# Kernel tuning notes

Hardware: AMD Instinct MI355X
Metric: run time of the kernel (lower is better)

Reference implementation:

```python
import jax, jax.numpy as jnp
import numpy as np

HIDDEN_DIM = 4096
NUM_EXPERTS = 64
TOP_K = 2
TEMPERATURE = 1.0
NUM_TOKENS = 16384


def setup_inputs() -> dict:
    key = jax.random.key(0)
    kx, kw = jax.random.split(key)
    x = jax.random.normal(kx, (NUM_TOKENS, HIDDEN_DIM), dtype=jnp.float32)
    # nn.Linear(hidden_dim, num_experts, bias=False): weight shape [num_experts, hidden_dim]
    W = jax.random.normal(kw, (NUM_EXPERTS, HIDDEN_DIM), dtype=jnp.float32) * (1.0 / np.sqrt(HIDDEN_DIM))
    return {"x": x, "W": W}


def reference(x, W):
    # gate linear: [N, H] @ [H, E] -> [N, E]
    logits = jnp.einsum("nh,eh->ne", x, W) / TEMPERATURE
    probs = jax.nn.softmax(logits, axis=-1)

    top_k_probs, top_k_indices = jax.lax.top_k(probs, TOP_K)  # [N, k]
    top_k_weights = top_k_probs / jnp.sum(top_k_probs, axis=-1, keepdims=True)

    # ---- stats (fused histogram instead of per-expert loop) ----
    expert_counts = jnp.zeros((NUM_EXPERTS,), dtype=jnp.float32).at[top_k_indices.ravel()].add(1.0)
    avg_probs = jnp.mean(probs, axis=0)
    entropy = jnp.mean(-jnp.sum(probs * jnp.log(probs + 1e-10), axis=-1))
    sorted_counts = jnp.sort(expert_counts)
    n = NUM_EXPERTS
    index = jnp.arange(1, n + 1, dtype=jnp.float32)
    gini = jnp.sum((2.0 * index - n - 1.0) * sorted_counts) / (n * jnp.sum(sorted_counts) + 1e-10)

    return (top_k_indices, top_k_weights, expert_counts, avg_probs, entropy, gini)
```

## Files before the change

### kernel.cpp

```cpp
#include <hip/hip_runtime.h>
#include <cstdint>
#include <cstddef>

#define NTOK 16384
#define HID  4096
#define NEXP 64
#define LO_SCALE 2048.0f
#define LO_INV   (1.0f/2048.0f)

typedef _Float16 half8  __attribute__((ext_vector_type(8)));
typedef _Float16 half4v __attribute__((ext_vector_type(4)));
typedef float    f32x4  __attribute__((ext_vector_type(4)));

__global__ __launch_bounds__(256) void wsplit_kernel(
    const float* __restrict__ W, _Float16* __restrict__ whi,
    _Float16* __restrict__ wlo) {
  int i = (blockIdx.x * 256 + threadIdx.x) * 4;
  float4 w = *(const float4*)(W + i);
  float f[4] = {w.x, w.y, w.z, w.w};
  half4v h, l;
#pragma unroll
  for (int j = 0; j < 4; ++j) {
    float hf = __uint_as_float(__float_as_uint(f[j]) & 0xffffe000u);
    h[j] = (_Float16)hf;
    l[j] = (_Float16)((f[j] - hf) * LO_SCALE);
  }
  *(half4v*)(whi + i) = h;
  *(half4v*)(wlo + i) = l;
}

__global__ __launch_bounds__(256, 2) void fused_kernel(
    const float* __restrict__ x, const _Float16* __restrict__ whi,
    const _Float16* __restrict__ wlo, float* __restrict__ out,
    float* __restrict__ gstats) {
  __shared__ float red[32][NEXP];
  __shared__ float savg[NEXP];
  __shared__ float scnt[NEXP];
  __shared__ float sent;

  const int tid     = threadIdx.x;
  const int lane    = tid & 63;
  const int wv      = tid >> 6;
  const int tokhalf = wv & 1;
  const int khalf   = wv >> 1;
  const int row     = lane & 15;
  const int g       = lane >> 4;

  if (tid < NEXP) { savg[tid] = 0.f; scnt[tid] = 0.f; }
  if (tid == 0) sent = 0.f;

  const int t0 = blockIdx.x * 32 + tokhalf * 16;
  const float*    xp  = x   + (size_t)(t0 + row) * HID + khalf * 2048 + g * 8;
  const _Float16* whp = whi + (size_t)row * HID        + khalf * 2048 + g * 8;
  const _Float16* wlp = wlo + (size_t)row * HID        + khalf * 2048 + g * 8;
  const size_t estride = (size_t)16 * HID;

  f32x4 acc[4], crs[4];
#pragma unroll
  for (int e = 0; e < 4; ++e) {
    acc[e] = (f32x4){0.f, 0.f, 0.f, 0.f};
    crs[e] = (f32x4){0.f, 0.f, 0.f, 0.f};
  }

#define LDA(KS, P0, P1)                              \
  P0 = *(const float4*)(xp + (KS) * 32);             \
  P1 = *(const float4*)(xp + (KS) * 32 + 4);

#define LDB(KS, BH, BL)                                        \
  _Pragma("unroll")                                            \
  for (int e = 0; e < 4; ++e) {                                \
    BH[e] = *(const half8*)(whp + e * estride + (KS) * 32);    \
    BL[e] = *(const half8*)(wlp + e * estride + (KS) * 32);    \
  }

#define STEP(P0, P1, BH, BL)                                              \
  {                                                                       \
    float ff[8] = {P0.x, P0.y, P0.z, P0.w, P1.x, P1.y, P1.z, P1.w};       \
    half8 ah, al;                                                         \
    _Pragma("unroll")                                                     \
    for (int j = 0; j < 8; ++j) {                                         \
      float hf = __uint_as_float(__float_as_uint(ff[j]) & 0xffffe000u);   \
      ah[j] = (_Float16)hf;                                               \
      al[j] = (_Float16)((ff[j] - hf) * LO_SCALE);                        \
    }                                                                     \
    _Pragma("unroll")                                                     \
    for (int e = 0; e < 4; ++e) {                                         \
      acc[e] = __builtin_amdgcn_mfma_f32_16x16x32_f16(ah, BH[e], acc[e], 0, 0, 0); \
      crs[e] = __builtin_amdgcn_mfma_f32_16x16x32_f16(ah, BL[e], crs[e], 0, 0, 0); \
      crs[e] = __builtin_amdgcn_mfma_f32_16x16x32_f16(al, BH[e], crs[e], 0, 0, 0); \
    }                                                                     \
  }

  float4 xa0, xa1, xb0, xb1;
  half8 bh0[4], bl0[4], bh1[4], bl1[4];

  LDA(0, xa0, xa1)
  LDB(0, bh0, bl0)
  for (int ks = 0; ks < 64; ks += 2) {
    LDA(ks + 1, xb0, xb1)
    LDB(ks + 1, bh1, bl1)
    STEP(xa0, xa1, bh0, bl0)
    if (ks + 2 < 64) {
      LDA(ks + 2, xa0, xa1)
      LDB(ks + 2, bh0, bl0)
    }
    STEP(xb0, xb1, bh1, bl1)
  }

  float v[4][4];
#pragma unroll
  for (int e = 0; e < 4; ++e)
#pragma unroll
    for (int r = 0; r < 4; ++r)
      v[e][r] = acc[e][r] + crs[e][r] * LO_INV;

  if (khalf == 1) {
#pragma unroll
    for (int e = 0; e < 4; ++e)
#pragma unroll
      for (int r = 0; r < 4; ++r)
        red[tokhalf * 16 + g * 4 + r][e * 16 + row] = v[e][r];
  }
  __syncthreads();

  if (khalf == 0) {
#pragma unroll
    for (int e = 0; e < 4; ++e)
#pragma unroll
      for (int r = 0; r < 4; ++r)
        v[e][r] += red[tokhalf * 16 + g * 4 + r][e * 16 + row];

    float m[4], S[4], PL[4];
#pragma unroll
    for (int r = 0; r < 4; ++r) {
      float mm = fmaxf(fmaxf(v[0][r], v[1][r]), fmaxf(v[2][r], v[3][r]));
#pragma unroll
      for (int off = 1; off < 16; off <<= 1) mm = fmaxf(mm, __shfl_xor(mm, off));
      m[r] = mm;
    }
    float p[4][4];
#pragma unroll
    for (int e = 0; e < 4; ++e)
#pragma unroll
      for (int r = 0; r < 4; ++r)
        p[e][r] = __expf(v[e][r] - m[r]);
#pragma unroll
    for (int r = 0; r < 4; ++r) {
      float s  = p[0][r] + p[1][r] + p[2][r] + p[3][r];
      float pl = p[0][r] * v[0][r] + p[1][r] * v[1][r] +
                 p[2][r] * v[2][r] + p[3][r] * v[3][r];
#pragma unroll
      for (int off = 1; off < 16; off <<= 1) {
        s  += __shfl_xor(s, off);
        pl += __shfl_xor(pl, off);
      }
      S[r] = s; PL[r] = pl;
    }

    float v1[4], v2[4]; int i1[4], i2[4];
#pragma unroll
    for (int r = 0; r < 4; ++r) {
      float a1 = -3.4e38f, a2 = -3.4e38f; int j1 = 0, j2 = 0;
#pragma unroll
      for (int e = 0; e < 4; ++e) {
        float val = v[e][r]; int idx = e * 16 + row;
        if (val > a1)      { a2 = a1; j2 = j1; a1 = val; j1 = idx; }
        else if (val > a2) { a2 = val; j2 = idx; }
      }
#pragma unroll
      for (int off = 1; off < 16; off <<= 1) {
        float o1 = __shfl_xor(a1, off), o2 = __shfl_xor(a2, off);
        int  oj1 = __shfl_xor(j1, off), oj2 = __shfl_xor(j2, off);
        if (o1 > a1 || (o1 == a1 && oj1 < j1)) {
          if (a1 > o2 || (a1 == o2 && j1 < oj2)) { a2 = a1; j2 = j1; }
          else                                   { a2 = o2; j2 = oj2; }
          a1 = o1; j1 = oj1;
        } else if (o1 > a2 || (o1 == a2 && oj1 < j2)) {
          a2 = o1; j2 = oj1;
        }
      }
      v1[r] = a1; v2[r] = a2; i1[r] = j1; i2[r] = j2;
    }

    float inv[4] = {1.f / S[0], 1.f / S[1], 1.f / S[2], 1.f / S[3]};

#pragma unroll
    for (int e = 0; e < 4; ++e) {
      float s = p[e][0] * inv[0] + p[e][1] * inv[1] +
                p[e][2] * inv[2] + p[e][3] * inv[3];
      s += __shfl_xor(s, 16);
      s += __shfl_xor(s, 32);
      if (lane < 16) atomicAdd(&savg[e * 16 + row], s);
    }

    if (row == 0) {
      float hsum = 0.f;
#pragma unroll
      for (int r = 0; r < 4; ++r) {
        hsum += m[r] + __logf(S[r]) - PL[r] * inv[r];
        atomicAdd(&scnt[i1[r]], 1.f);
        atomicAdd(&scnt[i2[r]], 1.f);
        int t = t0 + g * 4 + r;
        float e2 = __expf(v2[r] - v1[r]);
        float w1 = 1.f / (1.f + e2);
        out[2 * t]     = (float)i1[r];
        out[2 * t + 1] = (float)i2[r];
        out[2 * NTOK + 2 * t]     = w1;
        out[2 * NTOK + 2 * t + 1] = e2 * w1;
      }
      atomicAdd(&sent, hsum);
    }
  }
  __syncthreads();
  if (tid < NEXP) {
    atomicAdd(&gstats[tid],        scnt[tid]);
    atomicAdd(&gstats[NEXP + tid], savg[tid]);
  }
  if (tid == 0) atomicAdd(&gstats[2 * NEXP], sent);
}

__global__ void finalize_kernel(const float* __restrict__ gstats,
                                float* __restrict__ out) {
  const int e = threadIdx.x;
  const float c   = gstats[e];
  const float avg = gstats[NEXP + e] * (1.0f / NTOK);

  out[4 * NTOK + e]        = c;
  out[4 * NTOK + NEXP + e] = avg;

  __shared__ float cs[NEXP];
  cs[e] = c;
  __syncthreads();

  int rank = 0;
  for (int j = 0; j < NEXP; ++j) {
    float cj = cs[j];
    rank += (cj < c || (cj == c && j < e)) ? 1 : 0;
  }
  float val = (2.0f * (rank + 1) - NEXP - 1) * c;
  float tot = c;
#pragma unroll
  for (int off = 32; off; off >>= 1) {
    val += __shfl_xor(val, off);
    tot += __shfl_xor(tot, off);
  }
  if (e == 0) {
    out[4 * NTOK + 2 * NEXP]     = gstats[2 * NEXP] * (1.0f / NTOK);
    out[4 * NTOK + 2 * NEXP + 1] = val / (NEXP * tot + 1e-10f);
  }
}

extern "C" void kernel_launch(void* const* d_in, const int* in_sizes, int n_in,
                              void* d_out, int out_size, void* d_ws, size_t ws_size,
                              hipStream_t stream) {
  const float* x = (const float*)d_in[0];
  const float* W = (const float*)d_in[1];
  float* out = (float*)d_out;

  _Float16* whi = (_Float16*)d_ws;
  _Float16* wlo = whi + (size_t)NEXP * HID;
  float* gstats = (float*)(wlo + (size_t)NEXP * HID);

  hipMemsetAsync(gstats, 0, (2 * NEXP + 1) * sizeof(float), stream);
  wsplit_kernel<<<dim3((NEXP * HID) / (256 * 4)), 256, 0, stream>>>(W, whi, wlo);
  fused_kernel<<<dim3(NTOK / 32), 256, 0, stream>>>(x, whi, wlo, out, gstats);
  finalize_kernel<<<dim3(1), 64, 0, stream>>>(gstats, out);
}
```

Baseline: 460.7 us.

## Split K four ways per block and reuse each W fragment across two token tiles

Each wave now covers a quarter of the hidden dimension for all 32 tokens of the block, instead of half of K for 16 tokens. Each loaded W hi/lo fragment therefore feeds MFMAs for two 16-token tiles, which halves W load traffic per token. The loop is restructured into a deeper software pipeline: three x stages in flight and two W stages, unrolled by four. The cost is more accumulator and buffer registers, which may hurt occupancy at launch bounds (256,2), plus a three-way shared-memory reduction that uses padded rows to avoid bank conflicts.

```diff
diff --git a/kernel.cpp b/kernel.cpp
--- a/kernel.cpp
+++ b/kernel.cpp
@@ -29,186 +29,215 @@
   *(half4v*)(wlo + i) = l;
 }
 
+__device__ __forceinline__ void cvt_split(float4 p0, float4 p1,
+                                          half8& ah, half8& al) {
+  float ff[8] = {p0.x, p0.y, p0.z, p0.w, p1.x, p1.y, p1.z, p1.w};
+#pragma unroll
+  for (int j = 0; j < 8; ++j) {
+    float hf = __uint_as_float(__float_as_uint(ff[j]) & 0xffffe000u);
+    ah[j] = (_Float16)hf;
+    al[j] = (_Float16)((ff[j] - hf) * LO_SCALE);
+  }
+}
+
 __global__ __launch_bounds__(256, 2) void fused_kernel(
     const float* __restrict__ x, const _Float16* __restrict__ whi,
     const _Float16* __restrict__ wlo, float* __restrict__ out,
     float* __restrict__ gstats) {
-  __shared__ float red[32][NEXP];
+  __shared__ float red[3][32][65];
   __shared__ float savg[NEXP];
   __shared__ float scnt[NEXP];
   __shared__ float sent;
 
-  const int tid     = threadIdx.x;
-  const int lane    = tid & 63;
-  const int wv      = tid >> 6;
-  const int tokhalf = wv & 1;
-  const int khalf   = wv >> 1;
-  const int row     = lane & 15;
-  const int g       = lane >> 4;
+  const int tid  = threadIdx.x;
+  const int lane = tid & 63;
+  const int wv   = tid >> 6;
+  const int row  = lane & 15;
+  const int g    = lane >> 4;
 
   if (tid < NEXP) { savg[tid] = 0.f; scnt[tid] = 0.f; }
   if (tid == 0) sent = 0.f;
 
-  const int t0 = blockIdx.x * 32 + tokhalf * 16;
-  const float*    xp  = x   + (size_t)(t0 + row) * HID + khalf * 2048 + g * 8;
-  const _Float16* whp = whi + (size_t)row * HID        + khalf * 2048 + g * 8;
-  const _Float16* wlp = wlo + (size_t)row * HID        + khalf * 2048 + g * 8;
-  const size_t estride = (size_t)16 * HID;
-
-  f32x4 acc[4], crs[4];
+  const int t0 = blockIdx.x * 32;
+  const float*    xp0 = x   + (size_t)(t0 + row) * HID + wv * 1024 + g * 8;
+  const float*    xp1 = xp0 + (size_t)16 * HID;
+  const _Float16* whp = whi + (size_t)row * HID + wv * 1024 + g * 8;
+  const _Float16* wlp = wlo + (size_t)row * HID + wv * 1024 + g * 8;
+
+  f32x4 acc0[4], crs0[4], acc1[4], crs1[4];
 #pragma unroll
   for (int e = 0; e < 4; ++e) {
-    acc[e] = (f32x4){0.f, 0.f, 0.f, 0.f};
-    crs[e] = (f32x4){0.f, 0.f, 0.f, 0.f};
-  }
-
-#define LDA(KS, P0, P1)                              \
-  P0 = *(const float4*)(xp + (KS) * 32);             \
-  P1 = *(const float4*)(xp + (KS) * 32 + 4);
-
-#define LDB(KS, BH, BL)                                        \
-  _Pragma("unroll")                                            \
-  for (int e = 0; e < 4; ++e) {                                \
-    BH[e] = *(const half8*)(whp + e * estride + (KS) * 32);    \
-    BL[e] = *(const half8*)(wlp + e * estride + (KS) * 32);    \
-  }
-
-#define STEP(P0, P1, BH, BL)                                              \
-  {                                                                       \
-    float ff[8] = {P0.x, P0.y, P0.z, P0.w, P1.x, P1.y, P1.z, P1.w};       \
-    half8 ah, al;                                                         \
-    _Pragma("unroll")                                                     \
-    for (int j = 0; j < 8; ++j) {                                         \
-      float hf = __uint_as_float(__float_as_uint(ff[j]) & 0xffffe000u);   \
-      ah[j] = (_Float16)hf;                                               \
-      al[j] = (_Float16)((ff[j] - hf) * LO_SCALE);                        \
-    }                                                                     \
-    _Pragma("unroll")                                                     \
-    for (int e = 0; e < 4; ++e) {                                         \
-      acc[e] = __builtin_amdgcn_mfma_f32_16x16x32_f16(ah, BH[e], acc[e], 0, 0, 0); \
-      crs[e] = __builtin_amdgcn_mfma_f32_16x16x32_f16(ah, BL[e], crs[e], 0, 0, 0); \
-      crs[e] = __builtin_amdgcn_mfma_f32_16x16x32_f16(al, BH[e], crs[e], 0, 0, 0); \
-    }                                                                     \
-  }
-
-  float4 xa0, xa1, xb0, xb1;
-  half8 bh0[4], bl0[4], bh1[4], bl1[4];
-
-  LDA(0, xa0, xa1)
-  LDB(0, bh0, bl0)
-  for (int ks = 0; ks < 64; ks += 2) {
-    LDA(ks + 1, xb0, xb1)
-    LDB(ks + 1, bh1, bl1)
-    STEP(xa0, xa1, bh0, bl0)
-    if (ks + 2 < 64) {
-      LDA(ks + 2, xa0, xa1)
-      LDB(ks + 2, bh0, bl0)
+    acc0[e] = (f32x4){0.f,0.f,0.f,0.f}; crs0[e] = (f32x4){0.f,0.f,0.f,0.f};
+    acc1[e] = (f32x4){0.f,0.f,0.f,0.f}; crs1[e] = (f32x4){0.f,0.f,0.f,0.f};
+  }
+
+  float4 xb[4][4];
+  half8  wh[2][4], wl[2][4];
+
+#define XLD(ks, B) {                                   \
+    const int _o = (ks) * 32;                          \
+    xb[B][0] = *(const float4*)(xp0 + _o);             \
+    xb[B][1] = *(const float4*)(xp0 + _o + 4);         \
+    xb[B][2] = *(const float4*)(xp1 + _o);             \
+    xb[B][3] = *(const float4*)(xp1 + _o + 4);         \
+  }
+
+#define WLD(ks, B) {                                             \
+    const int _o = (ks) * 32;                                    \
+    _Pragma("unroll")                                            \
+    for (int e = 0; e < 4; ++e) {                                \
+      wh[B][e] = *(const half8*)(whp + e * 65536 + _o);          \
+      wl[B][e] = *(const half8*)(wlp + e * 65536 + _o);          \
+    }                                                            \
+  }
+
+#define STEP(XB, WB) {                                                        \
+    half8 ah0, al0, ah1, al1;                                                 \
+    cvt_split(xb[XB][0], xb[XB][1], ah0, al0);                                \
+    cvt_split(xb[XB][2], xb[XB][3], ah1, al1);                                \
+    _Pragma("unroll")                                                         \
+    for (int e = 0; e < 4; ++e) {                                             \
+      acc0[e] = __builtin_amdgcn_mfma_f32_16x16x32_f16(ah0, wh[WB][e], acc0[e], 0,0,0); \
+      crs0[e] = __builtin_amdgcn_mfma_f32_16x16x32_f16(ah0, wl[WB][e], crs0[e], 0,0,0); \
+      crs0[e] = __builtin_amdgcn_mfma_f32_16x16x32_f16(al0, wh[WB][e], crs0[e], 0,0,0); \
+      acc1[e] = __builtin_amdgcn_mfma_f32_16x16x32_f16(ah1, wh[WB][e], acc1[e], 0,0,0); \
+      crs1[e] = __builtin_amdgcn_mfma_f32_16x16x32_f16(ah1, wl[WB][e], crs1[e], 0,0,0); \
+      crs1[e] = __builtin_amdgcn_mfma_f32_16x16x32_f16(al1, wh[WB][e], crs1[e], 0,0,0); \
+    }                                                                         \
+  }
+
+  XLD(0, 0) XLD(1, 1) XLD(2, 2)
+  WLD(0, 0) WLD(1, 1)
+
+  for (int kk = 0; kk < 8; ++kk) {
+#pragma unroll
+    for (int u = 0; u < 4; ++u) {
+      const int K  = kk * 4 + u;
+      const int kx = (K + 3 < 32) ? K + 3 : 31;
+      const int kw = (K + 2 < 32) ? K + 2 : 31;
+      switch (u) {
+        case 0: STEP(0, 0) XLD(kx, 3) WLD(kw, 0) break;
+        case 1: STEP(1, 1) XLD(kx, 0) WLD(kw, 1) break;
+        case 2: STEP(2, 0) XLD(kx, 1) WLD(kw, 0) break;
+        default: STEP(3, 1) XLD(kx, 2) WLD(kw, 1) break;
+      }
     }
-    STEP(xb0, xb1, bh1, bl1)
-  }
-
-  float v[4][4];
+  }
+
+  float v[2][4][4];
 #pragma unroll
   for (int e = 0; e < 4; ++e)
 #pragma unroll
-    for (int r = 0; r < 4; ++r)
-      v[e][r] = acc[e][r] + crs[e][r] * LO_INV;
-
-  if (khalf == 1) {
-#pragma unroll
-    for (int e = 0; e < 4; ++e)
-#pragma unroll
-      for (int r = 0; r < 4; ++r)
-        red[tokhalf * 16 + g * 4 + r][e * 16 + row] = v[e][r];
+    for (int r = 0; r < 4; ++r) {
+      v[0][e][r] = acc0[e][r] + crs0[e][r] * LO_INV;
+      v[1][e][r] = acc1[e][r] + crs1[e][r] * LO_INV;
+    }
+
+  if (wv != 0) {
+#pragma unroll
+    for (int mt = 0; mt < 2; ++mt)
+#pragma unroll
+      for (int e = 0; e < 4; ++e)
+#pragma unroll
+        for (int r = 0; r < 4; ++r)
+          red[wv - 1][mt * 16 + g * 4 + r][e * 16 + row] = v[mt][e][r];
   }
   __syncthreads();
 
-  if (khalf == 0) {
-#pragma unroll
-    for (int e = 0; e < 4; ++e)
-#pragma unroll
-      for (int r = 0; r < 4; ++r)
-        v[e][r] += red[tokhalf * 16 + g * 4 + r][e * 16 + row];
-
-    float m[4], S[4], PL[4];
-#pragma unroll
-    for (int r = 0; r < 4; ++r) {
-      float mm = fmaxf(fmaxf(v[0][r], v[1][r]), fmaxf(v[2][r], v[3][r]));
-#pragma unroll
-      for (int off = 1; off < 16; off <<= 1) mm = fmaxf(mm, __shfl_xor(mm, off));
-      m[r] = mm;
-    }
-    float p[4][4];
-#pragma unroll
-    for (int e = 0; e < 4; ++e)
-#pragma unroll
-      for (int r = 0; r < 4; ++r)
-        p[e][r] = __expf(v[e][r] - m[r]);
-#pragma unroll
-    for (int r = 0; r < 4; ++r) {
-      float s  = p[0][r] + p[1][r] + p[2][r] + p[3][r];
-      float pl = p[0][r] * v[0][r] + p[1][r] * v[1][r] +
-                 p[2][r] * v[2][r] + p[3][r] * v[3][r];
-#pragma unroll
-      for (int off = 1; off < 16; off <<= 1) {
-        s  += __shfl_xor(s, off);
-        pl += __shfl_xor(pl, off);
-      }
-      S[r] = s; PL[r] = pl;
-    }
-
-    float v1[4], v2[4]; int i1[4], i2[4];
-#pragma unroll
-    for (int r = 0; r < 4; ++r) {
-      float a1 = -3.4e38f, a2 = -3.4e38f; int j1 = 0, j2 = 0;
+  if (wv == 0) {
+#pragma unroll
+    for (int mt = 0; mt < 2; ++mt)
+#pragma unroll
+      for (int e = 0; e < 4; ++e)
+#pragma unroll
+        for (int r = 0; r < 4; ++r) {
+          const int tr = mt * 16 + g * 4 + r, ec = e * 16 + row;
+          v[mt][e][r] += red[0][tr][ec] + red[1][tr][ec] + red[2][tr][ec];
+        }
+
+#pragma unroll
+    for (int mt = 0; mt < 2; ++mt) {
+      float m[4], S[4], PL[4];
+#pragma unroll
+      for (int r = 0; r < 4; ++r) {
+        float mm = fmaxf(fmaxf(v[mt][0][r], v[mt][1][r]),
+                         fmaxf(v[mt][2][r], v[mt][3][r]));
+#pragma unroll
+        for (int off = 1; off < 16; off <<= 1) mm = fmaxf(mm, __shfl_xor(mm, off));
+        m[r] = mm;
+      }
+      float p[4][4];
+#pragma unroll
+      for (int e = 0; e < 4; ++e)
+#pragma unroll
+        for (int r = 0; r < 4; ++r)
+          p[e][r] = __expf(v[mt][e][r] - m[r]);
+#pragma unroll
+      for (int r = 0; r < 4; ++r) {
+        float s  = p[0][r] + p[1][r] + p[2][r] + p[3][r];
+        float pl = p[0][r] * v[mt][0][r] + p[1][r] * v[mt][1][r] +
+                   p[2][r] * v[mt][2][r] + p[3][r] * v[mt][3][r];
+#pragma unroll
+        for (int off = 1; off < 16; off <<= 1) {
+          s  += __shfl_xor(s, off);
+          pl += __shfl_xor(pl, off);
+        }
+        S[r] = s; PL[r] = pl;
+      }
+
+      float v1[4], v2[4]; int i1[4], i2[4];
+#pragma unroll
+      for (int r = 0; r < 4; ++r) {
+        float a1 = -3.4e38f, a2 = -3.4e38f; int j1 = 0, j2 = 0;
+#pragma unroll
+        for (int e = 0; e < 4; ++e) {
+          float val = v[mt][e][r]; int idx = e * 16 + row;
+          if (val > a1)      { a2 = a1; j2 = j1; a1 = val; j1 = idx; }
+          else if (val > a2) { a2 = val; j2 = idx; }
+        }
+#pragma unroll
+        for (int off = 1; off < 16; off <<= 1) {
+          float o1 = __shfl_xor(a1, off), o2 = __shfl_xor(a2, off);
+          int  oj1 = __shfl_xor(j1, off), oj2 = __shfl_xor(j2, off);
+          if (o1 > a1 || (o1 == a1 && oj1 < j1)) {
+            if (a1 > o2 || (a1 == o2 && j1 < oj2)) { a2 = a1; j2 = j1; }
+            else                                   { a2 = o2; j2 = oj2; }
+            a1 = o1; j1 = oj1;
+          } else if (o1 > a2 || (o1 == a2 && oj1 < j2)) {
+            a2 = o1; j2 = oj1;
+          }
+        }
+        v1[r] = a1; v2[r] = a2; i1[r] = j1; i2[r] = j2;
+      }
+
+      float inv[4] = {1.f / S[0], 1.f / S[1], 1.f / S[2], 1.f / S[3]};
+
 #pragma unroll
       for (int e = 0; e < 4; ++e) {
-        float val = v[e][r]; int idx = e * 16 + row;
-        if (val > a1)      { a2 = a1; j2 = j1; a1 = val; j1 = idx; }
-        else if (val > a2) { a2 = val; j2 = idx; }
-      }
-#pragma unroll
-      for (int off = 1; off < 16; off <<= 1) {
-        float o1 = __shfl_xor(a1, off), o2 = __shfl_xor(a2, off);
-        int  oj1 = __shfl_xor(j1, off), oj2 = __shfl_xor(j2, off);
-        if (o1 > a1 || (o1 == a1 && oj1 < j1)) {
-          if (a1 > o2 || (a1 == o2 && j1 < oj2)) { a2 = a1; j2 = j1; }
-          else                                   { a2 = o2; j2 = oj2; }
-          a1 = o1; j1 = oj1;
-        } else if (o1 > a2 || (o1 == a2 && oj1 < j2)) {
-          a2 = o1; j2 = oj1;
-        }
-      }
-      v1[r] = a1; v2[r] = a2; i1[r] = j1; i2[r] = j2;
-    }
-
-    float inv[4] = {1.f / S[0], 1.f / S[1], 1.f / S[2], 1.f / S[3]};
-
-#pragma unroll
-    for (int e = 0; e < 4; ++e) {
-      float s = p[e][0] * inv[0] + p[e][1] * inv[1] +
-                p[e][2] * inv[2] + p[e][3] * inv[3];
-      s += __shfl_xor(s, 16);
-      s += __shfl_xor(s, 32);
-      if (lane < 16) atomicAdd(&savg[e * 16 + row], s);
-    }
-
-    if (row == 0) {
-      float hsum = 0.f;
-#pragma unroll
-      for (int r = 0; r < 4; ++r) {
-        hsum += m[r] + __logf(S[r]) - PL[r] * inv[r];
-        atomicAdd(&scnt[i1[r]], 1.f);
-        atomicAdd(&scnt[i2[r]], 1.f);
-        int t = t0 + g * 4 + r;
-        float e2 = __expf(v2[r] - v1[r]);
-        float w1 = 1.f / (1.f + e2);
-        out[2 * t]     = (float)i1[r];
-        out[2 * t + 1] = (float)i2[r];
-        out[2 * NTOK + 2 * t]     = w1;
-        out[2 * NTOK + 2 * t + 1] = e2 * w1;
-      }
-      atomicAdd(&sent, hsum);
+        float s = p[e][0] * inv[0] + p[e][1] * inv[1] +
+                  p[e][2] * inv[2] + p[e][3] * inv[3];
+        s += __shfl_xor(s, 16);
+        s += __shfl_xor(s, 32);
+        if (lane < 16) atomicAdd(&savg[e * 16 + row], s);
+      }
+
+      if (row == 0) {
+        float hsum = 0.f;
+#pragma unroll
+        for (int r = 0; r < 4; ++r) {
+          hsum += m[r] + __logf(S[r]) - PL[r] * inv[r];
+          atomicAdd(&scnt[i1[r]], 1.f);
+          atomicAdd(&scnt[i2[r]], 1.f);
+          int t = t0 + mt * 16 + g * 4 + r;
+          float e2 = __expf(v2[r] - v1[r]);
+          float w1 = 1.f / (1.f + e2);
+          out[2 * t]     = (float)i1[r];
+          out[2 * t + 1] = (float)i2[r];
+          out[2 * NTOK + 2 * t]     = w1;
+          out[2 * NTOK + 2 * t + 1] = e2 * w1;
+        }
+        atomicAdd(&sent, hsum);
+      }
     }
   }
   __syncthreads();
```

Measured after the change: 449.2 us. 2.5% less time.
